# Performance work log

Hardware: AMD Instinct MI355X
Metric: run time of the kernel (lower is better)

The kernel has to match this reference:

```python
import jax, jax.numpy as jnp
import numpy as np

N = 50000      # nodes
E = 800000     # edges
FEAT = 128     # input feature dim
EMB = 256      # embed_dim = heads * hid
H = 4          # attention heads
C = 64         # hid_dim per head
PED = 32       # positional encoding dim
NEG_SLOPE = 0.2


def setup_inputs() -> dict:
    key = jax.random.key(0)
    ks = jax.random.split(key, 20)
    s = lambda i, shape, sc=0.1: jax.random.normal(ks[i], shape, jnp.float32) * sc
    return {
        "x": s(0, (N, FEAT), 1.0),
        "x_masked": s(1, (N, FEAT), 1.0),
        "PE": s(2, (N, PED), 1.0),
        "PE_noise": s(3, (N, PED), 1.0),
        "edge_index": jax.random.randint(ks[4], (2, E), 0, N),
        # PEG positional encoder (linear + relu)
        "W_peg": s(5, (PED, PED)), "b_peg": jnp.zeros((PED,), jnp.float32),
        # GAT layer 0
        "W0": s(6, (FEAT, H * C)), "a_s0": s(7, (H, C)), "a_d0": s(8, (H, C)),
        "w_pe0": s(9, (H,)), "W_u0": s(10, (PED, PED)),
        # GAT layer 1
        "W1": s(11, (EMB, H * C)), "a_s1": s(12, (H, C)), "a_d1": s(13, (H, C)),
        "w_pe1": s(14, (H,)), "W_u1": s(15, (PED, PED)),
    }


def _gat(x, pe, src, dst, W, a_s, a_d, w_pe, W_u):
    # PE-aware GATConv: standard GAT attention + PE-distance bias per head.
    xp = (x @ W).reshape(-1, H, C)                       # [N,H,C]
    al_s = (xp * a_s).sum(-1)                            # [N,H]
    al_d = (xp * a_d).sum(-1)                            # [N,H]
    dist = jnp.sqrt(((pe[src] - pe[dst]) ** 2).sum(-1) + 1e-8)   # [E]
    logits = jax.nn.leaky_relu(al_s[src] + al_d[dst], NEG_SLOPE) \
             + dist[:, None] * w_pe                      # [E,H]
    # segment softmax over incoming edges of each dst node
    m = jax.ops.segment_max(logits, dst, num_segments=N)
    e = jnp.exp(logits - m[dst])
    den = jax.ops.segment_sum(e, dst, num_segments=N)
    alpha = e / (den[dst] + 1e-16)                       # [E,H]
    out = jax.ops.segment_sum(alpha[:, :, None] * xp[src], dst,
                              num_segments=N).reshape(-1, H * C)  # [N,H*C]
    pe_out = jax.nn.relu(pe @ W_u)                       # per-layer PE update
    return out, pe_out


def reference(x, x_masked, PE, PE_noise, W_peg, b_peg,
              W0, a_s0, a_d0, w_pe0, W_u0,
              W1, a_s1, a_d1, w_pe1, W_u1, edge_index):
    src, dst = edge_index[0], edge_index[1]
    # PEG encoder on both PE branches
    pe = jax.nn.relu(PE @ W_peg + b_peg)
    pe_n = jax.nn.relu(PE_noise @ W_peg + b_peg)
    # layer 0 (dual branches; eval mode -> dropout is identity)
    h, pe_n = _gat(x, pe_n, src, dst, W0, a_s0, a_d0, w_pe0, W_u0)
    hm, pe = _gat(x_masked, pe, src, dst, W0, a_s0, a_d0, w_pe0, W_u0)
    h = jax.nn.relu(h)
    hm = jax.nn.relu(hm)
    # layer 1 (last layer: no activation)
    h, pe_n = _gat(h, pe_n, src, dst, W1, a_s1, a_d1, w_pe1, W_u1)
    hm, pe = _gat(hm, pe, src, dst, W1, a_s1, a_d1, w_pe1, W_u1)
    return (hm, pe_n)
```

## Files before the change

### kernel.cpp

```cpp
#include <hip/hip_runtime.h>
#include <hip/hip_bf16.h>

#define N_NODES 50000
#define N_EDGES 800000
#define NEG_SLOPE 0.2f

typedef __hip_bfloat16 bf16;
typedef __attribute__((ext_vector_type(8))) short short8;
typedef __attribute__((ext_vector_type(4))) float f32x4;

__device__ __forceinline__ float b2f(bf16 x) { return __bfloat162float(x); }

__device__ __forceinline__ float ldsel(const void* p, size_t i, int isbf) {
  return isbf ? __bfloat162float(((const bf16*)p)[i]) : ((const float*)p)[i];
}
__device__ __forceinline__ void stsel(void* p, size_t i, int isbf, float v) {
  if (isbf) ((bf16*)p)[i] = __float2bfloat16(v);
  else ((float*)p)[i] = v;
}

__global__ void detect_kernel(const unsigned short* __restrict__ probe,
                              int* __restrict__ flag) {
  if (threadIdx.x == 0 && blockIdx.x == 0) {
    int weird = 0;
    for (int i = 0; i < 512; i += 2) {
      int ex = (probe[i] >> 7) & 0xFF;
      if (ex >= 0x85) weird++;
    }
    *flag = (weird < 8) ? 1 : 0;
  }
}

struct CvtJobs {
  const void* src[10];
  float* dst[10];
  int n[10];
};
__global__ __launch_bounds__(256) void cvt_kernel(CvtJobs jobs, const int* __restrict__ flag) {
  int isbf = *flag;
  for (int j = 0; j < 10; j++) {
    int n = jobs.n[j];
    const void* s = jobs.src[j];
    float* d = jobs.dst[j];
    for (int i = blockIdx.x * 256 + threadIdx.x; i < n; i += gridDim.x * 256)
      d[i] = ldsel(s, i, isbf);
  }
}

template <int K>
__global__ __launch_bounds__(256) void transpose_cvt_kernel(const void* __restrict__ in,
                                                            bf16* __restrict__ out,
                                                            const int* __restrict__ flag) {
  int isbf = *flag;
  int i = blockIdx.x * 256 + threadIdx.x;
  if (i >= 256 * K) return;
  int n = i / K, k = i - n * K;
  out[i] = __float2bfloat16(ldsel(in, (size_t)k * 256 + n, isbf));
}

__global__ __launch_bounds__(256) void peg_chain3(const void* __restrict__ in,
                                                  const float* __restrict__ Wpeg,
                                                  const float* __restrict__ bpeg,
                                                  const float* __restrict__ Wu0,
                                                  const float* __restrict__ Wu1,
                                                  void* out, size_t out_off,
                                                  const int* __restrict__ flag) {
  __shared__ float w1[1024], w2[1024], w3[1024];
  __shared__ float rowA[256], rowB[256];
  int isbf = *flag;
  int tid = threadIdx.x;
  int n0 = blockIdx.x * 8;
  for (int i = tid; i < 1024; i += 256) {
    w1[i] = Wpeg[i];
    w2[i] = Wu0[i];
    w3[i] = Wu1[i];
  }
  rowA[tid] = ldsel(in, (size_t)n0 * 32 + tid, isbf);
  __syncthreads();
  int col = tid & 31, ln = tid >> 5;
  float acc = bpeg[col];
#pragma unroll
  for (int j = 0; j < 32; j++) acc += rowA[ln * 32 + j] * w1[j * 32 + col];
  rowB[tid] = fmaxf(acc, 0.f);
  __syncthreads();
  acc = 0.f;
#pragma unroll
  for (int j = 0; j < 32; j++) acc += rowB[ln * 32 + j] * w2[j * 32 + col];
  rowA[tid] = fmaxf(acc, 0.f);
  __syncthreads();
  acc = 0.f;
#pragma unroll
  for (int j = 0; j < 32; j++) acc += rowA[ln * 32 + j] * w3[j * 32 + col];
  stsel(out, out_off + (size_t)n0 * 32 + tid, isbf, fmaxf(acc, 0.f));
}

__global__ __launch_bounds__(256) void peg_chain2(const void* __restrict__ in,
                                                  const float* __restrict__ Wpeg,
                                                  const float* __restrict__ bpeg,
                                                  const float* __restrict__ Wu0,
                                                  bf16* __restrict__ pe0,
                                                  bf16* __restrict__ pe1,
                                                  const int* __restrict__ flag) {
  __shared__ float w1[1024], w2[1024];
  __shared__ float rowA[256], rowB[256];
  int isbf = *flag;
  int tid = threadIdx.x;
  int n0 = blockIdx.x * 8;
  for (int i = tid; i < 1024; i += 256) {
    w1[i] = Wpeg[i];
    w2[i] = Wu0[i];
  }
  rowA[tid] = ldsel(in, (size_t)n0 * 32 + tid, isbf);
  __syncthreads();
  int col = tid & 31, ln = tid >> 5;
  float acc = bpeg[col];
#pragma unroll
  for (int j = 0; j < 32; j++) acc += rowA[ln * 32 + j] * w1[j * 32 + col];
  acc = fmaxf(acc, 0.f);
  pe0[(size_t)n0 * 32 + tid] = __float2bfloat16(acc);
  rowB[tid] = acc;
  __syncthreads();
  acc = 0.f;
#pragma unroll
  for (int j = 0; j < 32; j++) acc += rowB[ln * 32 + j] * w2[j * 32 + col];
  pe1[(size_t)n0 * 32 + tid] = __float2bfloat16(fmaxf(acc, 0.f));
}

template <int K, bool A_DUAL>
__global__ __launch_bounds__(256) void mfma_gemm(const void* __restrict__ Ap,
                                                 const bf16* __restrict__ Bt,
                                                 bf16* __restrict__ C, int M,
                                                 const float* __restrict__ a_sf,
                                                 const float* __restrict__ a_df,
                                                 float* __restrict__ al_s,
                                                 float* __restrict__ al_d,
                                                 const int* __restrict__ flag) {
  constexpr int LDK = 136;
  __shared__ short a_lds[64 * LDK];
  __shared__ short b_lds[64 * LDK];
  __shared__ float lds_al[128];
  int isbf = A_DUAL ? *flag : 1;
  int tid = threadIdx.x;
  int row0 = blockIdx.x * 64;
  int col0 = blockIdx.y * 64;
  int lane = tid & 63;
  int wv = tid >> 6;
  int wm = (wv & 1) * 32, wn = (wv >> 1) * 32;
  int l15 = lane & 15, quad = lane >> 4;
  if (tid < 128) lds_al[tid] = 0.f;
  f32x4 acc00 = {0.f, 0.f, 0.f, 0.f}, acc01 = acc00, acc10 = acc00, acc11 = acc00;

  for (int kb = 0; kb < K; kb += 128) {
    if (kb) __syncthreads();
    for (int idx = tid; idx < 64 * 16; idx += 256) {
      int r = idx >> 4, sidx = idx & 15;
      int gr = row0 + r;
      size_t gi = (size_t)gr * K + kb + sidx * 8;
      uint4 av = make_uint4(0u, 0u, 0u, 0u);
      if (A_DUAL && !isbf) {
        if (gr < M) {
          float4 f0 = ((const float4*)Ap)[gi / 4];
          float4 f1 = ((const float4*)Ap)[gi / 4 + 1];
          union { uint4 v; bf16 h[8]; } o;
          o.h[0] = __float2bfloat16(f0.x);
          o.h[1] = __float2bfloat16(f0.y);
          o.h[2] = __float2bfloat16(f0.z);
          o.h[3] = __float2bfloat16(f0.w);
          o.h[4] = __float2bfloat16(f1.x);
          o.h[5] = __float2bfloat16(f1.y);
          o.h[6] = __float2bfloat16(f1.z);
          o.h[7] = __float2bfloat16(f1.w);
          av = o.v;
        }
      } else {
        if (gr < M) av = *(const uint4*)&((const bf16*)Ap)[gi];
      }
      *(uint4*)&a_lds[r * LDK + sidx * 8] = av;
      *(uint4*)&b_lds[r * LDK + sidx * 8] =
          *(const uint4*)&Bt[(size_t)(col0 + r) * K + kb + sidx * 8];
    }
    __syncthreads();
#pragma unroll
    for (int k0 = 0; k0 < 128; k0 += 32) {
      int ko = k0 + quad * 8;
      short8 a0 = *(const short8*)&a_lds[(wm + l15) * LDK + ko];
      short8 a1 = *(const short8*)&a_lds[(wm + 16 + l15) * LDK + ko];
      short8 b0 = *(const short8*)&b_lds[(wn + l15) * LDK + ko];
      short8 b1 = *(const short8*)&b_lds[(wn + 16 + l15) * LDK + ko];
      acc00 = __builtin_amdgcn_mfma_f32_16x16x32_bf16(a0, b0, acc00, 0, 0, 0);
      acc01 = __builtin_amdgcn_mfma_f32_16x16x32_bf16(a0, b1, acc01, 0, 0, 0);
      acc10 = __builtin_amdgcn_mfma_f32_16x16x32_bf16(a1, b0, acc10, 0, 0, 0);
      acc11 = __builtin_amdgcn_mfma_f32_16x16x32_bf16(a1, b1, acc11, 0, 0, 0);
    }
  }
  const f32x4* accs[2][2] = {{&acc00, &acc01}, {&acc10, &acc11}};
  float as0 = a_sf[col0 + wn + l15], as1 = a_sf[col0 + wn + 16 + l15];
  float ad0 = a_df[col0 + wn + l15], ad1 = a_df[col0 + wn + 16 + l15];
#pragma unroll
  for (int i = 0; i < 2; i++) {
    float sp[4], dp[4];
#pragma unroll
    for (int r = 0; r < 4; r++) {
      float v0 = (*accs[i][0])[r], v1 = (*accs[i][1])[r];
      sp[r] = v0 * as0 + v1 * as1;
      dp[r] = v0 * ad0 + v1 * ad1;
      int grow = row0 + wm + i * 16 + quad * 4 + r;
      if (grow < M) {
        C[(size_t)grow * 256 + col0 + wn + l15] = __float2bfloat16(v0);
        C[(size_t)grow * 256 + col0 + wn + 16 + l15] = __float2bfloat16(v1);
      }
    }
#pragma unroll
    for (int off = 1; off < 16; off <<= 1) {
#pragma unroll
      for (int r = 0; r < 4; r++) {
        sp[r] += __shfl_xor(sp[r], off);
        dp[r] += __shfl_xor(dp[r], off);
      }
    }
    if (l15 == 0) {
#pragma unroll
      for (int r = 0; r < 4; r++) {
        int lrow = wm + i * 16 + quad * 4 + r;
        atomicAdd(&lds_al[lrow], sp[r]);
        atomicAdd(&lds_al[64 + lrow], dp[r]);
      }
    }
  }
  __syncthreads();
  if (tid < 64 && row0 + tid < M) {
    al_s[(size_t)(row0 + tid) * 4 + blockIdx.y] = lds_al[tid];
    al_d[(size_t)(row0 + tid) * 4 + blockIdx.y] = lds_al[64 + tid];
  }
}

__global__ __launch_bounds__(256) void hist_kernel(const int* __restrict__ dst,
                                                   int* __restrict__ deg) {
  int e = blockIdx.x * 256 + threadIdx.x;
  atomicAdd(&deg[dst[e]], 1);
}

__global__ __launch_bounds__(1024) void scan1_kernel(const int* __restrict__ deg,
                                                     int* __restrict__ tmp,
                                                     int* __restrict__ bsum, int n) {
  __shared__ int wsum[16];
  int tid = threadIdx.x;
  int idx = blockIdx.x * 1024 + tid;
  int v = (idx < n) ? deg[idx] : 0;
  int incl = v;
#pragma unroll
  for (int off = 1; off < 64; off <<= 1) {
    int t = __shfl_up(incl, off);
    if ((tid & 63) >= off) incl += t;
  }
  int wid = tid >> 6;
  if ((tid & 63) == 63) wsum[wid] = incl;
  __syncthreads();
  if (tid == 0) {
    int acc = 0;
#pragma unroll
    for (int w = 0; w < 16; w++) {
      int t = wsum[w];
      wsum[w] = acc;
      acc += t;
    }
    bsum[blockIdx.x] = acc;
  }
  __syncthreads();
  if (idx < n) tmp[idx] = wsum[wid] + incl;
}

__global__ void scan2_kernel(int* __restrict__ bsum, int nb) {
  int tid = threadIdx.x;
  int v = (tid < nb) ? bsum[tid] : 0;
  int incl = v;
#pragma unroll
  for (int off = 1; off < 64; off <<= 1) {
    int t = __shfl_up(incl, off);
    if (tid >= off) incl += t;
  }
  if (tid < nb) bsum[tid] = incl - v;
}

__global__ __launch_bounds__(1024) void scan3_kernel(const int* __restrict__ tmp,
                                                     const int* __restrict__ bsum,
                                                     int* __restrict__ rowptr, int n) {
  int idx = blockIdx.x * 1024 + threadIdx.x;
  if (idx < n) rowptr[idx + 1] = tmp[idx] + bsum[blockIdx.x];
  if (idx == 0) rowptr[0] = 0;
}

__global__ __launch_bounds__(256) void fill_kernel(const int* __restrict__ src,
                                                   const int* __restrict__ dst,
                                                   const int* __restrict__ rowptr,
                                                   int* __restrict__ fill,
                                                   int* __restrict__ csr_src) {
  int e = blockIdx.x * 256 + threadIdx.x;
  int d = dst[e];
  int pos = atomicAdd(&fill[d], 1);
  csr_src[rowptr[d] + pos] = src[e];
}

template <bool RELU, bool OUT_DUAL>
__global__ __launch_bounds__(256) void agg_kernel(const bf16* __restrict__ xp,
                                                  const bf16* __restrict__ pe,
                                                  const float* __restrict__ al_s,
                                                  const float* __restrict__ al_d,
                                                  const float* __restrict__ w_pe,
                                                  const int* __restrict__ csr_src,
                                                  const int* __restrict__ rowptr,
                                                  void* out, const int* __restrict__ flag) {
  int isbf = OUT_DUAL ? *flag : 1;
  int lane = threadIdx.x & 63;
  int n = blockIdx.x * 4 + (threadIdx.x >> 6);
  int q = lane >> 4, li = lane & 15, h = li >> 2;
  unsigned int ud = *(const unsigned int*)&pe[(size_t)n * 32 + li * 2];
  float pdlo = __uint_as_float(ud << 16);
  float pdhi = __uint_as_float(ud & 0xffff0000u);
  float ald = al_d[(size_t)n * 4 + h];
  float wph = w_pe[h];
  int s1 = rowptr[n + 1];
  int s = rowptr[n] + q;
  float acc[16];
#pragma unroll
  for (int j = 0; j < 16; j++) acc[j] = 0.f;
  float asum = 0.f;
  int sn = -1;
  unsigned int pes = 0;
  float als = 0.f;
  if (s < s1) {
    sn = csr_src[s];
    pes = *(const unsigned int*)&pe[(size_t)sn * 32 + li * 2];
    als = al_s[(size_t)sn * 4 + h];
  }
  while (sn >= 0) {
    int s2 = s + 4;
    int sn2 = -1;
    unsigned int pes2 = 0;
    float als2 = 0.f;
    if (s2 < s1) {
      sn2 = csr_src[s2];
      pes2 = *(const unsigned int*)&pe[(size_t)sn2 * 32 + li * 2];
      als2 = al_s[(size_t)sn2 * 4 + h];
    }
    const uint4* base = (const uint4*)&xp[(size_t)sn * 256 + li * 16];
    uint4 v0 = base[0];
    uint4 v1 = base[1];
    float dx = __uint_as_float(pes << 16) - pdlo;
    float dy = __uint_as_float(pes & 0xffff0000u) - pdhi;
    float d2 = dx * dx + dy * dy;
#pragma unroll
    for (int off = 1; off < 16; off <<= 1) d2 += __shfl_xor(d2, off);
    float lg = als + ald;
    lg = (lg >= 0.f) ? lg : NEG_SLOPE * lg;
    lg += sqrtf(d2 + 1e-8f) * wph;
    float a = __expf(lg);
    unsigned int u[8] = {v0.x, v0.y, v0.z, v0.w, v1.x, v1.y, v1.z, v1.w};
#pragma unroll
    for (int p = 0; p < 8; p++) {
      acc[2 * p] += a * __uint_as_float(u[p] << 16);
      acc[2 * p + 1] += a * __uint_as_float(u[p] & 0xffff0000u);
    }
    asum += a;
    s = s2;
    sn = sn2;
    pes = pes2;
    als = als2;
  }
#pragma unroll
  for (int j = 0; j < 16; j++) {
    acc[j] += __shfl_xor(acc[j], 16);
    acc[j] += __shfl_xor(acc[j], 32);
  }
  asum += __shfl_xor(asum, 16);
  asum += __shfl_xor(asum, 32);
  if (q == 0) {
    float inv = 1.f / (asum + 1e-16f);
    size_t oi = (size_t)n * 256 + li * 16;
    if (OUT_DUAL && !isbf) {
      float* of = (float*)out;
#pragma unroll
      for (int p = 0; p < 4; p++) {
        float4 f;
        f.x = acc[4 * p] * inv;
        f.y = acc[4 * p + 1] * inv;
        f.z = acc[4 * p + 2] * inv;
        f.w = acc[4 * p + 3] * inv;
        if (RELU) {
          f.x = fmaxf(f.x, 0.f);
          f.y = fmaxf(f.y, 0.f);
          f.z = fmaxf(f.z, 0.f);
          f.w = fmaxf(f.w, 0.f);
        }
        *(float4*)&of[oi + 4 * p] = f;
      }
    } else {
      union { uint4 v[2]; bf16 hh[16]; } o;
#pragma unroll
      for (int j = 0; j < 16; j++) {
        float r = acc[j] * inv;
        if (RELU) r = fmaxf(r, 0.f);
        o.hh[j] = __float2bfloat16(r);
      }
      uint4* ob = (uint4*)&((bf16*)out)[oi];
      ob[0] = o.v[0];
      ob[1] = o.v[1];
    }
  }
}

extern "C" void kernel_launch(void* const* d_in, const int* in_sizes, int n_in,
                              void* d_out, int out_size, void* d_ws, size_t ws_size,
                              hipStream_t stream) {
  const void* x_masked = d_in[1];
  const void* PE = d_in[2];
  const void* PE_noise = d_in[3];
  const int* ei = (const int*)d_in[4];
  const int* src = ei;
  const int* dst = ei + N_EDGES;

  char* w = (char*)d_ws;
  auto alloc = [&](size_t bytes) -> char* {
    char* p = w;
    w += (bytes + 255) / 256 * 256;
    return p;
  };
  int* flag = (int*)alloc(4);
  float* W_peg_f = (float*)alloc(1024 * 4);
  float* b_peg_f = (float*)alloc(32 * 4);
  float* a_s0_f = (float*)alloc(256 * 4);
  float* a_d0_f = (float*)alloc(256 * 4);
  float* w_pe0_f = (float*)alloc(4 * 4);
  float* W_u0_f = (float*)alloc(1024 * 4);
  float* a_s1_f = (float*)alloc(256 * 4);
  float* a_d1_f = (float*)alloc(256 * 4);
  float* w_pe1_f = (float*)alloc(4 * 4);
  float* W_u1_f = (float*)alloc(1024 * 4);
  bf16* Wt0 = (bf16*)alloc(32768 * 2);
  bf16* Wt1 = (bf16*)alloc(65536 * 2);
  bf16* pe0_bf = (bf16*)alloc((size_t)N_NODES * 32 * 2);
  bf16* pe1_bf = (bf16*)alloc((size_t)N_NODES * 32 * 2);
  float* al_s = (float*)alloc((size_t)N_NODES * 4 * 4);
  float* al_d = (float*)alloc((size_t)N_NODES * 4 * 4);
  int* degfill = (int*)alloc((size_t)N_NODES * 2 * 4);
  int* deg = degfill;
  int* fill = degfill + N_NODES;
  int* rowptr = (int*)alloc((size_t)(N_NODES + 1) * 4);
  int* stmp = (int*)alloc((size_t)N_NODES * 4);
  int* bsum = (int*)alloc(64 * 4);
  int* csr_src = (int*)alloc((size_t)N_EDGES * 4);
  bf16* xp = (bf16*)alloc((size_t)N_NODES * 256 * 2);
  bf16* hm0 = (bf16*)alloc((size_t)N_NODES * 256 * 2);

  detect_kernel<<<1, 64, 0, stream>>>((const unsigned short*)d_in[5], flag);
  CvtJobs jobs;
  int ji = 0;
  auto addjob = [&](const void* s, float* d, int n) {
    jobs.src[ji] = s; jobs.dst[ji] = d; jobs.n[ji] = n; ji++;
  };
  addjob(d_in[5], W_peg_f, 1024);
  addjob(d_in[6], b_peg_f, 32);
  addjob(d_in[8], a_s0_f, 256);
  addjob(d_in[9], a_d0_f, 256);
  addjob(d_in[10], w_pe0_f, 4);
  addjob(d_in[11], W_u0_f, 1024);
  addjob(d_in[13], a_s1_f, 256);
  addjob(d_in[14], a_d1_f, 256);
  addjob(d_in[15], w_pe1_f, 4);
  addjob(d_in[16], W_u1_f, 1024);
  cvt_kernel<<<16, 256, 0, stream>>>(jobs, flag);
  transpose_cvt_kernel<128><<<128, 256, 0, stream>>>(d_in[7], Wt0, flag);
  transpose_cvt_kernel<256><<<256, 256, 0, stream>>>(d_in[12], Wt1, flag);

  hipMemsetAsync(degfill, 0, (size_t)N_NODES * 2 * 4, stream);

  hist_kernel<<<N_EDGES / 256, 256, 0, stream>>>(dst, deg);
  scan1_kernel<<<49, 1024, 0, stream>>>(deg, stmp, bsum, N_NODES);
  scan2_kernel<<<1, 64, 0, stream>>>(bsum, 49);
  scan3_kernel<<<49, 1024, 0, stream>>>(stmp, bsum, rowptr, N_NODES);
  fill_kernel<<<N_EDGES / 256, 256, 0, stream>>>(src, dst, rowptr, fill, csr_src);

  peg_chain3<<<N_NODES / 8, 256, 0, stream>>>(PE_noise, W_peg_f, b_peg_f, W_u0_f, W_u1_f,
                                              d_out, (size_t)N_NODES * 256, flag);
  peg_chain2<<<N_NODES / 8, 256, 0, stream>>>(PE, W_peg_f, b_peg_f, W_u0_f, pe0_bf, pe1_bf, flag);

  {
    dim3 g((N_NODES + 63) / 64, 4);
    mfma_gemm<128, true><<<g, 256, 0, stream>>>(x_masked, Wt0, xp, N_NODES,
                                                a_s0_f, a_d0_f, al_s, al_d, flag);
  }
  agg_kernel<true, false><<<N_NODES / 4, 256, 0, stream>>>(
      xp, pe0_bf, al_s, al_d, w_pe0_f, csr_src, rowptr, hm0, flag);

  {
    dim3 g((N_NODES + 63) / 64, 4);
    mfma_gemm<256, false><<<g, 256, 0, stream>>>(hm0, Wt1, xp, N_NODES,
                                                 a_s1_f, a_d1_f, al_s, al_d, flag);
  }
  agg_kernel<false, true><<<N_NODES / 4, 256, 0, stream>>>(
      xp, pe1_bf, al_s, al_d, w_pe1_f, csr_src, rowptr, d_out, flag);
}
```

Before: 470.3 us.

## Remap GEMM blocks across XCDs and deepen agg gather prefetch pipeline

```diff
diff --git a/kernel.cpp b/kernel.cpp
--- a/kernel.cpp
+++ b/kernel.cpp
@@ -139,10 +139,17 @@
   __shared__ short a_lds[64 * LDK];
   __shared__ short b_lds[64 * LDK];
   __shared__ float lds_al[128];
+  int nrt = (M + 63) / 64;
+  int bid = blockIdx.x;
+  int xcd = bid & 7;
+  int jj = bid >> 3;
+  int col_t = jj & 3;
+  int row_t = (jj >> 2) * 8 + xcd;
+  if (row_t >= nrt) return;
   int isbf = A_DUAL ? *flag : 1;
   int tid = threadIdx.x;
-  int row0 = blockIdx.x * 64;
-  int col0 = blockIdx.y * 64;
+  int row0 = row_t * 64;
+  int col0 = col_t * 64;
   int lane = tid & 63;
   int wv = tid >> 6;
   int wm = (wv & 1) * 32, wn = (wv >> 1) * 32;
@@ -229,8 +236,8 @@
   }
   __syncthreads();
   if (tid < 64 && row0 + tid < M) {
-    al_s[(size_t)(row0 + tid) * 4 + blockIdx.y] = lds_al[tid];
-    al_d[(size_t)(row0 + tid) * 4 + blockIdx.y] = lds_al[64 + tid];
+    al_s[(size_t)(row0 + tid) * 4 + col_t] = lds_al[tid];
+    al_d[(size_t)(row0 + tid) * 4 + col_t] = lds_al[64 + tid];
   }
 }
 
@@ -325,47 +332,54 @@
 #pragma unroll
   for (int j = 0; j < 16; j++) acc[j] = 0.f;
   float asum = 0.f;
-  int sn = -1;
-  unsigned int pes = 0;
-  float als = 0.f;
+
+  int sn_c = -1, sn_n = -1;
+  unsigned int pes_c = 0, pes_n = 0;
+  float als_c = 0.f, als_n = 0.f;
+  uint4 xc0 = make_uint4(0u, 0u, 0u, 0u), xc1 = xc0;
+  uint4 xn0 = xc0, xn1 = xc0;
   if (s < s1) {
-    sn = csr_src[s];
-    pes = *(const unsigned int*)&pe[(size_t)sn * 32 + li * 2];
-    als = al_s[(size_t)sn * 4 + h];
-  }
-  while (sn >= 0) {
-    int s2 = s + 4;
-    int sn2 = -1;
-    unsigned int pes2 = 0;
-    float als2 = 0.f;
-    if (s2 < s1) {
-      sn2 = csr_src[s2];
-      pes2 = *(const unsigned int*)&pe[(size_t)sn2 * 32 + li * 2];
-      als2 = al_s[(size_t)sn2 * 4 + h];
-    }
-    const uint4* base = (const uint4*)&xp[(size_t)sn * 256 + li * 16];
-    uint4 v0 = base[0];
-    uint4 v1 = base[1];
-    float dx = __uint_as_float(pes << 16) - pdlo;
-    float dy = __uint_as_float(pes & 0xffff0000u) - pdhi;
+    sn_c = csr_src[s];
+    pes_c = *(const unsigned int*)&pe[(size_t)sn_c * 32 + li * 2];
+    als_c = al_s[(size_t)sn_c * 4 + h];
+    const uint4* b = (const uint4*)&xp[(size_t)sn_c * 256 + li * 16];
+    xc0 = b[0];
+    xc1 = b[1];
+    if (s + 4 < s1) sn_n = csr_src[s + 4];
+  }
+  int sf = s + 8;
+  while (sn_c >= 0) {
+    if (sn_n >= 0) {
+      pes_n = *(const unsigned int*)&pe[(size_t)sn_n * 32 + li * 2];
+      als_n = al_s[(size_t)sn_n * 4 + h];
+      const uint4* b = (const uint4*)&xp[(size_t)sn_n * 256 + li * 16];
+      xn0 = b[0];
+      xn1 = b[1];
+    }
+    int sn_f = (sf < s1) ? csr_src[sf] : -1;
+    sf += 4;
+    float dx = __uint_as_float(pes_c << 16) - pdlo;
+    float dy = __uint_as_float(pes_c & 0xffff0000u) - pdhi;
     float d2 = dx * dx + dy * dy;
 #pragma unroll
     for (int off = 1; off < 16; off <<= 1) d2 += __shfl_xor(d2, off);
-    float lg = als + ald;
+    float lg = als_c + ald;
     lg = (lg >= 0.f) ? lg : NEG_SLOPE * lg;
     lg += sqrtf(d2 + 1e-8f) * wph;
     float a = __expf(lg);
-    unsigned int u[8] = {v0.x, v0.y, v0.z, v0.w, v1.x, v1.y, v1.z, v1.w};
+    unsigned int u[8] = {xc0.x, xc0.y, xc0.z, xc0.w, xc1.x, xc1.y, xc1.z, xc1.w};
 #pragma unroll
     for (int p = 0; p < 8; p++) {
       acc[2 * p] += a * __uint_as_float(u[p] << 16);
       acc[2 * p + 1] += a * __uint_as_float(u[p] & 0xffff0000u);
     }
     asum += a;
-    s = s2;
-    sn = sn2;
-    pes = pes2;
-    als = als2;
+    sn_c = sn_n;
+    pes_c = pes_n;
+    als_c = als_n;
+    xc0 = xn0;
+    xc1 = xn1;
+    sn_n = sn_f;
   }
 #pragma unroll
   for (int j = 0; j < 16; j++) {
@@ -484,19 +498,16 @@
                                               d_out, (size_t)N_NODES * 256, flag);
   peg_chain2<<<N_NODES / 8, 256, 0, stream>>>(PE, W_peg_f, b_peg_f, W_u0_f, pe0_bf, pe1_bf, flag);
 
-  {
-    dim3 g((N_NODES + 63) / 64, 4);
-    mfma_gemm<128, true><<<g, 256, 0, stream>>>(x_masked, Wt0, xp, N_NODES,
-                                                a_s0_f, a_d0_f, al_s, al_d, flag);
-  }
+  int nrt = (N_NODES + 63) / 64;
+  int gblk = ((nrt + 7) / 8) * 8 * 4;
+
+  mfma_gemm<128, true><<<gblk, 256, 0, stream>>>(x_masked, Wt0, xp, N_NODES,
+                                                 a_s0_f, a_d0_f, al_s, al_d, flag);
   agg_kernel<true, false><<<N_NODES / 4, 256, 0, stream>>>(
       xp, pe0_bf, al_s, al_d, w_pe0_f, csr_src, rowptr, hm0, flag);
 
-  {
-    dim3 g((N_NODES + 63) / 64, 4);
-    mfma_gemm<256, false><<<g, 256, 0, stream>>>(hm0, Wt1, xp, N_NODES,
-                                                 a_s1_f, a_d1_f, al_s, al_d, flag);
-  }
+  mfma_gemm<256, false><<<gblk, 256, 0, stream>>>(hm0, Wt1, xp, N_NODES,
+                                                  a_s1_f, a_d1_f, al_s, al_d, flag);
   agg_kernel<false, true><<<N_NODES / 4, 256, 0, stream>>>(
       xp, pe1_bf, al_s, al_d, w_pe1_f, csr_src, rowptr, d_out, flag);
 }
```

Measured after the change: 470.3 us. Within noise of the previous version (-0.0%).
